# Kernel optimization log

Hardware: AMD Instinct MI355X
Metric: run time of the kernel (lower is better)

## Reference

```python
import jax, jax.numpy as jnp
import numpy as np

GROUPS = 32
EPS = 1e-5


def group_norm(x, gamma, beta):
    # x: [B,H,W,C], channels_last, groups over channel dim (Keras GroupNormalization default)
    B, H, W, C = x.shape
    xg = x.reshape(B, H, W, GROUPS, C // GROUPS)
    mean = xg.mean(axis=(1, 2, 4), keepdims=True)
    var = xg.var(axis=(1, 2, 4), keepdims=True)
    xn = ((xg - mean) * jax.lax.rsqrt(var + EPS)).reshape(B, H, W, C)
    return xn * gamma + beta


def conv1x1(x, w, b):
    # 1x1 conv == per-pixel dense: [B,H,W,C] x [C,D] -> [B,H,W,D]
    return jnp.einsum('bhwc,cd->bhwd', x, w) + b


def setup_inputs() -> dict:
    key = jax.random.key(0)
    ks = jax.random.split(key, 10)
    C = 512
    s = 1.0 / np.sqrt(C)
    inp = {
        'x': jax.random.normal(ks[0], (2, 64, 64, C), dtype=jnp.float32),
        'gamma': jnp.ones((C,), jnp.float32),
        'beta': jnp.zeros((C,), jnp.float32),
        'wq': jax.random.normal(ks[1], (C, C), jnp.float32) * s,
        'bq': jnp.zeros((C,), jnp.float32),
        'wk': jax.random.normal(ks[2], (C, C), jnp.float32) * s,
        'bk': jnp.zeros((C,), jnp.float32),
        'wv': jax.random.normal(ks[3], (C, C), jnp.float32) * s,
        'bv': jnp.zeros((C,), jnp.float32),
        'wp': jax.random.normal(ks[4], (C, C), jnp.float32) * s,
        'bp': jnp.zeros((C,), jnp.float32),
    }
    return inp


def reference(x, gamma, beta, wq, bq, wk, bk, wv, bv, wp, bp):
    B, H, W, C = x.shape
    N = H * W
    xn = group_norm(x, gamma, beta)
    q = conv1x1(xn, wq, bq).reshape(B, N, C)
    k = conv1x1(xn, wk, bk).reshape(B, N, C)
    v = conv1x1(xn, wv, bv).reshape(B, N, C)
    scale = 1.0 / jnp.sqrt(jnp.asarray(C, x.dtype))
    scores = jnp.einsum('bnc,bmc->bnm', q, k) * scale  # [B,N,N]
    attn = jax.nn.softmax(scores, axis=-1)
    out = jnp.einsum('bnm,bmc->bnc', attn, v).reshape(B, H, W, C)
    return conv1x1(out, wp, bp) + x
```

## Files before the change

kernel.cpp:

```cpp
#include <hip/hip_runtime.h>
#include <hip/hip_fp16.h>

typedef _Float16 half_t;
typedef _Float16 half8 __attribute__((ext_vector_type(8)));
typedef float floatx4 __attribute__((ext_vector_type(4)));

static constexpr int BATCH = 2;
static constexpr int NSP = 4096;
static constexpr int CH = 512;
static constexpr int NQKV = 3 * CH;
static constexpr int KSPLIT = 4;

static constexpr size_t OFF_STATS = 0;
static constexpr size_t OFF_ROWSUM = 512;
static constexpr size_t OFF_PST = 33280;
static constexpr size_t OFF_WQKV = 196608;
static constexpr size_t WQKV_BYTES = (size_t)NQKV * CH * 2;
static constexpr size_t OFF_WP = OFF_WQKV + WQKV_BYTES;
static constexpr size_t WP_BYTES = (size_t)CH * CH * 2;
static constexpr size_t OFF_XN = OFF_WP + WP_BYTES;
static constexpr size_t XN_BYTES = (size_t)BATCH * NSP * CH * 2;
static constexpr size_t OFF_QKV = OFF_XN + XN_BYTES;
static constexpr size_t QKV_BYTES = (size_t)BATCH * NSP * NQKV * 2;
static constexpr size_t OFF_VT = OFF_QKV + QKV_BYTES;
static constexpr size_t OFF_AO = OFF_VT + XN_BYTES;
static constexpr size_t OFF_S = OFF_AO + XN_BYTES;
static constexpr size_t S_BYTES_1 = (size_t)NSP * NSP * 2;
static constexpr size_t OFF_PART = OFF_XN;

__device__ __forceinline__ void gld16(void* lds, const void* g) {
  __builtin_amdgcn_global_load_lds(
      (__attribute__((address_space(1))) void*)(g),
      (__attribute__((address_space(3))) void*)(lds),
      16, 0, 0);
}

__global__ __launch_bounds__(256) void gn_stats(const float* __restrict__ x,
                                                float* __restrict__ pst) {
  int b = blockIdx.y;
  int tid = (int)threadIdx.x;
  int g = ((tid * 4) & (CH - 1)) >> 4;
  const float* base = x + (long)b * NSP * CH + (long)blockIdx.x * 16 * CH + tid * 4;
  float s = 0.f, s2 = 0.f;
#pragma unroll
  for (int it = 0; it < 8; ++it) {
    floatx4 v = *(const floatx4*)(base + (long)it * 1024);
#pragma unroll
    for (int r = 0; r < 4; ++r) { s += v[r]; s2 += v[r] * v[r]; }
  }
  __shared__ float gs[32], gs2[32];
  if (tid < 32) { gs[tid] = 0.f; gs2[tid] = 0.f; }
  __syncthreads();
  atomicAdd(&gs[g], s);
  atomicAdd(&gs2[g], s2);
  __syncthreads();
  if (tid < 32) {
    long idx = ((long)(b * 256 + blockIdx.x) * 32 + tid) * 2;
    pst[idx] = gs[tid];
    pst[idx + 1] = gs2[tid];
  }
}

__global__ __launch_bounds__(256) void gn_finalize(const float* __restrict__ pst,
                                                   float* __restrict__ st,
                                                   float* __restrict__ rowsum) {
  int tid = (int)threadIdx.x;
  int bg = tid & 63;
  int p = tid >> 6;
  int b = bg >> 5, g = bg & 31;
  float s = 0.f, s2 = 0.f;
  for (int j = 0; j < 64; ++j) {
    int chunk = p * 64 + j;
    long idx = ((long)(b * 256 + chunk) * 32 + g) * 2;
    s += pst[idx];
    s2 += pst[idx + 1];
  }
  __shared__ float rs[64][4], rs2[64][4];
  rs[bg][p] = s;
  rs2[bg][p] = s2;
  __syncthreads();
  if (tid < 64) {
    float ts = rs[tid][0] + rs[tid][1] + rs[tid][2] + rs[tid][3];
    float ts2 = rs2[tid][0] + rs2[tid][1] + rs2[tid][2] + rs2[tid][3];
    const float inv = 1.f / 65536.f;
    float mean = ts * inv;
    float var = ts2 * inv - mean * mean;
    st[tid * 2] = mean;
    st[tid * 2 + 1] = rsqrtf(var + 1e-5f);
  }
  floatx4* rz = (floatx4*)rowsum;
#pragma unroll
  for (int j = 0; j < 8; ++j)
    rz[tid + j * 256] = floatx4{0.f, 0.f, 0.f, 0.f};
}

__global__ __launch_bounds__(256) void gn_apply(const float* __restrict__ x,
                                                const float* __restrict__ st,
                                                const float* __restrict__ gamma,
                                                const float* __restrict__ beta,
                                                half_t* __restrict__ xn) {
  long i = ((long)blockIdx.x * 256 + threadIdx.x) * 8;
  int c = (int)(i & (CH - 1));
  int b = (int)(i >> 21);
  int g = c >> 4;
  float mean = st[((b << 5) + g) * 2];
  float rstd = st[((b << 5) + g) * 2 + 1];
  floatx4 a = *(const floatx4*)(x + i);
  floatx4 d = *(const floatx4*)(x + i + 4);
  half8 o;
#pragma unroll
  for (int r = 0; r < 4; ++r) {
    o[r]     = (half_t)((a[r] - mean) * rstd * gamma[c + r] + beta[c + r]);
    o[r + 4] = (half_t)((d[r] - mean) * rstd * gamma[c + r + 4] + beta[c + r + 4]);
  }
  *(half8*)(xn + i) = o;
}

__global__ __launch_bounds__(256) void transpose_w(
    const float* __restrict__ w0, const float* __restrict__ w1,
    const float* __restrict__ w2, const float* __restrict__ w3,
    half_t* __restrict__ o0, half_t* __restrict__ o1,
    half_t* __restrict__ o2, half_t* __restrict__ o3) {
  const float* w; half_t* o;
  switch (blockIdx.z) {
    case 0: w = w0; o = o0; break;
    case 1: w = w1; o = o1; break;
    case 2: w = w2; o = o2; break;
    default: w = w3; o = o3; break;
  }
  __shared__ float t[32][33];
  int d0 = blockIdx.x * 32, c0 = blockIdx.y * 32;
  int tx = threadIdx.x & 31, ty = threadIdx.x >> 5;
#pragma unroll
  for (int i = 0; i < 4; ++i)
    t[ty + i * 8][tx] = w[(long)(c0 + ty + i * 8) * CH + d0 + tx];
  __syncthreads();
#pragma unroll
  for (int i = 0; i < 4; ++i) {
    int d = ty + i * 8;
    o[(long)(d0 + d) * CH + c0 + tx] = (half_t)t[tx][d];
  }
}

__global__ __launch_bounds__(256) void transpose_v(const half_t* __restrict__ v,
                                                   half_t* __restrict__ vt) {
  __shared__ half_t t[32][33];
  int b = blockIdx.z;
  int d0 = blockIdx.x * 32, n0 = blockIdx.y * 32;
  int tx = threadIdx.x & 31, ty = threadIdx.x >> 5;
  const half_t* vb = v + (long)b * NSP * NQKV;
  half_t* ob = vt + (long)b * NSP * CH;
#pragma unroll
  for (int i = 0; i < 4; ++i)
    t[ty + i * 8][tx] = vb[(long)(n0 + ty + i * 8) * NQKV + d0 + tx];
  __syncthreads();
#pragma unroll
  for (int i = 0; i < 4; ++i) {
    int d = ty + i * 8;
    ob[(long)(d0 + d) * NSP + n0 + tx] = t[tx][d];
  }
}

template <int BM, int BN, int BK, int EPI, int SWZ, int KSP, typename OutT>
__global__ __launch_bounds__(256) void gemm_nt(
    const half_t* __restrict__ X, const half_t* __restrict__ Y,
    OutT* __restrict__ Co, const float* __restrict__ b0,
    const float* __restrict__ b1, const float* __restrict__ b2,
    const float* __restrict__ resid, float* __restrict__ rowsum,
    int M, int N, int K, int ldx, int ldy, int ldc,
    long xbs, long ybs, long cbs, float scale) {
  constexpr int SM = BM / 32;
  constexpr int SN = BN / 32;
  constexpr int ROWS = BM + BN;
  constexpr int CPR = BK / 8;
  constexpr int RPW = 64 / CPR;
  constexpr int ROUNDS = (ROWS * BK * 2) / 4096;
  constexpr int KSTEPS = BK / 32;
  static_assert(BM % (4 * RPW) == 0, "no As/Bs straddle within a round");
  __shared__ __align__(16) half_t Sh[ROWS * BK];

  const int zb = blockIdx.z / KSP;
  const int ks = blockIdx.z % KSP;
  int bx, by;
  if (SWZ == 1) {
    int lin = (int)(blockIdx.x + gridDim.x * blockIdx.y);
    int wmt = 256 / (int)gridDim.x;
    by = wmt * (lin >> 8) + ((lin & 255) % wmt);
    bx = (lin & 255) / wmt;
  } else if (SWZ == 2) {
    by = blockIdx.x;
    bx = blockIdx.y;
  } else {
    bx = blockIdx.x;
    by = blockIdx.y;
  }

  const half_t* Xb = X + (long)zb * xbs + (long)ks * K;
  const half_t* Yb = Y + (long)zb * ybs + (long)ks * K;
  OutT* Cb = Co + (long)blockIdx.z * cbs;

  const int m0 = by * BM;
  const int n0 = bx * BN;
  const int tid = (int)threadIdx.x;
  const int wave = tid >> 6;
  const int lane = tid & 63;
  const int quad = lane >> 4;
  const int l16 = lane & 15;
  const int wm = wave >> 1;
  const int wn = wave & 1;

  floatx4 acc[SM][SN] = {};

  const int srow = lane / CPR;
  const int schunk = lane % CPR;
  const char* Xc = (const char*)Xb;

  int soff[ROUNDS];
#pragma unroll
  for (int r = 0; r < ROUNDS; ++r) {
    int row = r * (4 * RPW) + wave * RPW + srow;
    int gchunk = schunk ^ (row & (CPR - 1));
    const char* p = (row < BM)
        ? (const char*)(Xb + (long)(m0 + row) * ldx)
        : (const char*)(Yb + (long)(n0 + row - BM) * ldy);
    soff[r] = (int)(p + gchunk * 16 - Xc);
  }

  int offA[SM], offB[SN];
#pragma unroll
  for (int i = 0; i < SM; ++i) {
    int m = wm * (BM / 2) + i * 16 + l16;
    int cc = quad ^ (m & (CPR - 1));
    offA[i] = (m * BK + cc * 8) * 2;
  }
#pragma unroll
  for (int j = 0; j < SN; ++j) {
    int n = wn * (BN / 2) + j * 16 + l16;
    int cc = quad ^ (n & (CPR - 1));
    offB[j] = (BM * BK + n * BK + cc * 8) * 2;
  }

  for (int k0 = 0; k0 < K; k0 += BK) {
#pragma unroll
    for (int r = 0; r < ROUNDS; ++r) {
      gld16((char*)Sh + (r * 4 + wave) * 1024, Xc + (long)soff[r]);
      soff[r] += BK * 2;
    }
    __syncthreads();

#pragma unroll
    for (int kk = 0; kk < KSTEPS; ++kk) {
      const int kx = kk << 6;
      half8 af[SM], bf[SN];
#pragma unroll
      for (int i = 0; i < SM; ++i)
        af[i] = *(const half8*)((const char*)Sh + (offA[i] ^ kx));
#pragma unroll
      for (int j = 0; j < SN; ++j)
        bf[j] = *(const half8*)((const char*)Sh + (offB[j] ^ kx));
#pragma unroll
      for (int i = 0; i < SM; ++i)
#pragma unroll
        for (int j = 0; j < SN; ++j)
          acc[i][j] = __builtin_amdgcn_mfma_f32_16x16x32_f16(af[i], bf[j], acc[i][j], 0, 0, 0);
    }
    __syncthreads();
  }

#pragma unroll
  for (int i = 0; i < SM; ++i) {
    int gmb = m0 + wm * (BM / 2) + i * 16 + quad * 4;
    float rs[4] = {0.f, 0.f, 0.f, 0.f};
#pragma unroll
    for (int j = 0; j < SN; ++j) {
      int gn = n0 + wn * (BN / 2) + j * 16 + l16;
      float bias = 0.f, sc = 1.f;
      if (EPI == 1) {
        if (gn < CH) { bias = b0[gn]; sc = scale; }
        else if (gn < 2 * CH) { bias = b1[gn - CH]; }
        else { bias = b2[gn - 2 * CH]; }
      } else if (EPI == 2) {
        bias = b0[gn];
      }
#pragma unroll
      for (int r = 0; r < 4; ++r) {
        long idx = (long)(gmb + r) * ldc + gn;
        float v = acc[i][j][r];
        if (EPI == 1) v = (v + bias) * sc;
        if (EPI == 2) v = v + bias + resid[idx];
        if (EPI == 3) { v = __expf(v); rs[r] += v; }
        Cb[idx] = (OutT)v;
      }
    }
    if (EPI == 3) {
#pragma unroll
      for (int r = 0; r < 4; ++r) {
        float v = rs[r];
        v += __shfl_xor(v, 1);
        v += __shfl_xor(v, 2);
        v += __shfl_xor(v, 4);
        v += __shfl_xor(v, 8);
        if (l16 == 0) atomicAdd(&rowsum[(long)zb * NSP + gmb + r], v);
      }
    }
  }
}

__global__ __launch_bounds__(256) void pv_combine(const half_t* __restrict__ part,
                                                  const float* __restrict__ rowsum,
                                                  half_t* __restrict__ ao) {
  const long bNC = (long)NSP * CH;
  long i = ((long)blockIdx.x * 256 + threadIdx.x) * 8;
  int b = (int)(i >> 21);
  long inner = i & ((1L << 21) - 1);
  float inv = 1.f / rowsum[i >> 9];
  float s[8] = {};
#pragma unroll
  for (int ks = 0; ks < KSPLIT; ++ks) {
    half8 h = *(const half8*)(part + ((long)(b * KSPLIT + ks)) * bNC + inner);
#pragma unroll
    for (int r = 0; r < 8; ++r) s[r] += (float)h[r];
  }
  half8 o;
#pragma unroll
  for (int r = 0; r < 8; ++r) o[r] = (half_t)(s[r] * inv);
  *(half8*)(ao + i) = o;
}

extern "C" void kernel_launch(void* const* d_in, const int* in_sizes, int n_in,
                              void* d_out, int out_size, void* d_ws, size_t ws_size,
                              hipStream_t stream) {
  const float* x = (const float*)d_in[0];
  const float* gamma = (const float*)d_in[1];
  const float* beta = (const float*)d_in[2];
  const float* wq = (const float*)d_in[3];
  const float* bq = (const float*)d_in[4];
  const float* wk = (const float*)d_in[5];
  const float* bk = (const float*)d_in[6];
  const float* wv = (const float*)d_in[7];
  const float* bv = (const float*)d_in[8];
  const float* wp = (const float*)d_in[9];
  const float* bp = (const float*)d_in[10];
  float* out = (float*)d_out;
  char* ws = (char*)d_ws;

  float* st = (float*)(ws + OFF_STATS);
  float* rsum = (float*)(ws + OFF_ROWSUM);
  float* pst = (float*)(ws + OFF_PST);
  half_t* wqkvT = (half_t*)(ws + OFF_WQKV);
  half_t* wpT = (half_t*)(ws + OFF_WP);
  half_t* xn = (half_t*)(ws + OFF_XN);
  half_t* qkv = (half_t*)(ws + OFF_QKV);
  half_t* vt = (half_t*)(ws + OFF_VT);
  half_t* ao = (half_t*)(ws + OFF_AO);
  half_t* S = (half_t*)(ws + OFF_S);
  half_t* part = (half_t*)(ws + OFF_PART);

  half_t* q = qkv;
  half_t* k = qkv + CH;
  half_t* v = qkv + 2 * CH;

  const float scale = 0.044194173824159216f;
  const long bQKV = (long)NSP * NQKV;
  const long bNC = (long)NSP * CH;
  const long bNN = (long)NSP * NSP;

  gn_stats<<<dim3(256, BATCH), 256, 0, stream>>>(x, pst);
  gn_finalize<<<1, 256, 0, stream>>>(pst, st, rsum);
  gn_apply<<<2048, 256, 0, stream>>>(x, st, gamma, beta, xn);
  transpose_w<<<dim3(16, 16, 4), 256, 0, stream>>>(
      wq, wk, wv, wp, wqkvT, wqkvT + (size_t)CH * CH, wqkvT + 2 * (size_t)CH * CH, wpT);

  gemm_nt<128, 128, 64, 1, 2, 1, half_t><<<dim3(BATCH * NSP / 128, NQKV / 128, 1), 256, 0, stream>>>(
      xn, wqkvT, qkv, bq, bk, bv, nullptr, nullptr, BATCH * NSP, NQKV, CH,
      CH, CH, NQKV, 0, 0, 0, scale);
  transpose_v<<<dim3(16, 128, BATCH), 256, 0, stream>>>(v, vt);

  bool full = ws_size >= OFF_S + 2 * S_BYTES_1;
  if (full) {
    gemm_nt<128, 128, 64, 3, 1, 1, half_t><<<dim3(32, 32, BATCH), 256, 0, stream>>>(
        q, k, S, nullptr, nullptr, nullptr, nullptr, rsum, NSP, NSP, CH,
        NQKV, NQKV, NSP, bQKV, bQKV, bNN, 1.f);
    gemm_nt<128, 128, 64, 0, 2, KSPLIT, half_t><<<dim3(NSP / 128, CH / 128, BATCH * KSPLIT), 256, 0, stream>>>(
        S, vt, part, nullptr, nullptr, nullptr, nullptr, nullptr, NSP, CH, NSP / KSPLIT,
        NSP, NSP, CH, bNN, bNC, bNC, 1.f);
    pv_combine<<<2048, 256, 0, stream>>>(part, rsum, ao);
  } else {
    for (int bb = 0; bb < BATCH; ++bb) {
      gemm_nt<128, 128, 64, 3, 1, 1, half_t><<<dim3(32, 32, 1), 256, 0, stream>>>(
          q + bb * bQKV, k + bb * bQKV, S, nullptr, nullptr, nullptr, nullptr,
          rsum + bb * NSP, NSP, NSP, CH, NQKV, NQKV, NSP, 0, 0, 0, 1.f);
      gemm_nt<128, 128, 64, 0, 2, KSPLIT, half_t><<<dim3(NSP / 128, CH / 128, KSPLIT), 256, 0, stream>>>(
          S, vt + bb * bNC, part + (long)bb * KSPLIT * bNC, nullptr, nullptr, nullptr,
          nullptr, nullptr, NSP, CH, NSP / KSPLIT, NSP, NSP, CH, 0, 0, bNC, 1.f);
    }
    pv_combine<<<2048, 256, 0, stream>>>(part, rsum, ao);
  }
  gemm_nt<64, 64, 128, 2, 2, 1, float><<<dim3(BATCH * NSP / 64, CH / 64, 1), 256, 0, stream>>>(
      ao, wpT, out, bp, nullptr, nullptr, x, nullptr, BATCH * NSP, CH, CH,
      CH, CH, CH, 0, 0, 0, 1.f);
}
```

Before: 257.3 us.

## Add 256x256 eight-wave pipelined GEMM for attention QK and PV stages

Adds a new GEMM kernel with 256x256 tiles, 512 threads and a 128 KB LDS double buffer. Direct global-to-LDS loads are interleaved with MFMA phases, controlled by explicit vmcnt waits, barriers and setprio. The QK^T (with exp and rowsum epilogue) and split-K PV GEMMs now use it instead of the 128x128 kernel. The aim is more data reuse per tile and better overlap of loads with compute. In exchange, fewer blocks are launched, LDS use is very large, and the hand-tuned wait counts must be exactly right to stay correct.

```diff
diff --git a/kernel.cpp b/kernel.cpp
--- a/kernel.cpp
+++ b/kernel.cpp
@@ -34,6 +34,13 @@
       (__attribute__((address_space(3))) void*)(lds),
       16, 0, 0);
 }
+
+#define VMCNT(n) asm volatile("s_waitcnt vmcnt(" #n ")" ::: "memory")
+#define LGKM0()                                         \
+  do {                                                  \
+    asm volatile("s_waitcnt lgkmcnt(0)" ::: "memory");  \
+    __builtin_amdgcn_sched_barrier(0);                  \
+  } while (0)
 
 __global__ __launch_bounds__(256) void gn_stats(const float* __restrict__ x,
                                                 float* __restrict__ pst) {
@@ -306,6 +313,157 @@
   }
 }
 
+template <int EPI, int KSP, typename OutT>
+__global__ __launch_bounds__(512, 2) void gemm8p(
+    const half_t* __restrict__ X, const half_t* __restrict__ Y,
+    OutT* __restrict__ Co, float* __restrict__ rowsum,
+    int K, int ldx, int ldy, int ldc, long xbs, long ybs, long cbs) {
+  __shared__ __align__(16) char smem[131072];
+  const int zb = (int)blockIdx.z / KSP;
+  const int ks = (int)blockIdx.z % KSP;
+  const int m0 = (int)blockIdx.x * 256;
+  const int n0 = (int)blockIdx.y * 256;
+  const int tid = (int)threadIdx.x;
+  const int w = tid >> 6;
+  const int l = tid & 63;
+  const int quad = l >> 4;
+  const int l16 = l & 15;
+  const int wm = w >> 2;
+  const int wn = w & 3;
+
+  const half_t* Xb = X + (long)zb * xbs + (long)ks * K;
+  const half_t* Yb = Y + (long)zb * ybs + (long)ks * K;
+  OutT* Cb = Co + (long)blockIdx.z * cbs;
+  const char* Xc = (const char*)Xb;
+
+  int soff[8];
+  {
+    const int lr = l >> 3;
+    const int g = (l & 7) ^ (lr & 7);
+#pragma unroll
+    for (int r = 0; r < 8; ++r) {
+      const int R = (r * 8 + w) * 8 + lr;
+      const char* p = (R < 256)
+          ? (const char*)(Xb + (long)(m0 + R) * ldx)
+          : (const char*)(Yb + (long)(n0 + R - 256) * ldy);
+      soff[r] = (int)(p + g * 16 - Xc);
+    }
+  }
+
+  int offA[8], offB[4];
+#pragma unroll
+  for (int i = 0; i < 8; ++i) {
+    const int m = wm * 128 + i * 16 + l16;
+    offA[i] = m * 128 + ((quad ^ (m & 7)) << 4);
+  }
+#pragma unroll
+  for (int j = 0; j < 4; ++j) {
+    const int n = wn * 64 + j * 16 + l16;
+    offB[j] = 32768 + n * 128 + ((quad ^ (n & 7)) << 4);
+  }
+
+  floatx4 acc[8][4] = {};
+
+#pragma unroll
+  for (int r = 0; r < 8; ++r) {
+    gld16(smem + (r * 8 + w) * 1024, Xc + (long)soff[r]);
+    soff[r] += 128;
+  }
+  {
+    constexpr int pr[6] = {4, 5, 6, 7, 0, 2};
+#pragma unroll
+    for (int t = 0; t < 6; ++t) {
+      gld16(smem + 65536 + (pr[t] * 8 + w) * 1024, Xc + (long)soff[pr[t]]);
+      soff[pr[t]] += 128;
+    }
+  }
+  VMCNT(6);
+  __builtin_amdgcn_s_barrier();
+
+  const int NI = K >> 7;
+  half8 bf[4][2];
+  for (int it = 0; it < NI; ++it) {
+    const bool last = (it == NI - 1);
+    constexpr int sr0[8] = {1, 4, 6, 0, 1, 4, 6, 0};
+    constexpr int sr1[8] = {3, 5, 7, 2, 3, 5, 7, 2};
+    constexpr int spar[8] = {1, 0, 0, 0, 0, 1, 1, 1};
+#pragma unroll
+    for (int ph = 0; ph < 8; ++ph) {
+      const int q = ph & 3;
+      const char* bb = smem + (ph >> 2) * 65536;
+      if (q == 0) {
+#pragma unroll
+        for (int j = 0; j < 4; ++j)
+#pragma unroll
+          for (int kk = 0; kk < 2; ++kk)
+            bf[j][kk] = *(const half8*)(bb + (offB[j] ^ (kk << 6)));
+      }
+      half8 af[2][2];
+#pragma unroll
+      for (int i2 = 0; i2 < 2; ++i2)
+#pragma unroll
+        for (int kk = 0; kk < 2; ++kk)
+          af[i2][kk] = *(const half8*)(bb + (offA[q * 2 + i2] ^ (kk << 6)));
+      if (ph == 0 || !last) {
+        const int r0 = sr0[ph], r1 = sr1[ph];
+        char* db = smem + spar[ph] * 65536;
+        gld16(db + (r0 * 8 + w) * 1024, Xc + (long)soff[r0]);
+        soff[r0] += 128;
+        gld16(db + (r1 * 8 + w) * 1024, Xc + (long)soff[r1]);
+        soff[r1] += 128;
+      }
+      __builtin_amdgcn_s_barrier();
+      LGKM0();
+      __builtin_amdgcn_s_setprio(1);
+#pragma unroll
+      for (int i2 = 0; i2 < 2; ++i2)
+#pragma unroll
+        for (int j = 0; j < 4; ++j)
+#pragma unroll
+          for (int kk = 0; kk < 2; ++kk)
+            acc[q * 2 + i2][j] = __builtin_amdgcn_mfma_f32_16x16x32_f16(
+                af[i2][kk], bf[j][kk], acc[q * 2 + i2][j], 0, 0, 0);
+      __builtin_amdgcn_s_setprio(0);
+      if (ph == 3) {
+        if (last) { VMCNT(2); } else { VMCNT(8); }
+      } else if (ph == 5) {
+        if (last) { VMCNT(0); } else { VMCNT(10); }
+      } else if (ph == 7) {
+        if (!last) { VMCNT(6); }
+      }
+      __builtin_amdgcn_s_barrier();
+    }
+  }
+
+#pragma unroll
+  for (int i = 0; i < 8; ++i) {
+    const int gmb = m0 + wm * 128 + i * 16 + quad * 4;
+    float rs[4] = {0.f, 0.f, 0.f, 0.f};
+#pragma unroll
+    for (int j = 0; j < 4; ++j) {
+      const int gn = n0 + wn * 64 + j * 16 + l16;
+#pragma unroll
+      for (int r = 0; r < 4; ++r) {
+        long idx = (long)(gmb + r) * ldc + gn;
+        float v = acc[i][j][r];
+        if (EPI == 3) { v = __expf(v); rs[r] += v; }
+        Cb[idx] = (OutT)v;
+      }
+    }
+    if (EPI == 3) {
+#pragma unroll
+      for (int r = 0; r < 4; ++r) {
+        float v = rs[r];
+        v += __shfl_xor(v, 1);
+        v += __shfl_xor(v, 2);
+        v += __shfl_xor(v, 4);
+        v += __shfl_xor(v, 8);
+        if (l16 == 0) atomicAdd(&rowsum[(long)zb * NSP + gmb + r], v);
+      }
+    }
+  }
+}
+
 __global__ __launch_bounds__(256) void pv_combine(const half_t* __restrict__ part,
                                                   const float* __restrict__ rowsum,
                                                   half_t* __restrict__ ao) {
@@ -378,21 +536,19 @@
 
   bool full = ws_size >= OFF_S + 2 * S_BYTES_1;
   if (full) {
-    gemm_nt<128, 128, 64, 3, 1, 1, half_t><<<dim3(32, 32, BATCH), 256, 0, stream>>>(
-        q, k, S, nullptr, nullptr, nullptr, nullptr, rsum, NSP, NSP, CH,
-        NQKV, NQKV, NSP, bQKV, bQKV, bNN, 1.f);
-    gemm_nt<128, 128, 64, 0, 2, KSPLIT, half_t><<<dim3(NSP / 128, CH / 128, BATCH * KSPLIT), 256, 0, stream>>>(
-        S, vt, part, nullptr, nullptr, nullptr, nullptr, nullptr, NSP, CH, NSP / KSPLIT,
-        NSP, NSP, CH, bNN, bNC, bNC, 1.f);
+    gemm8p<3, 1, half_t><<<dim3(NSP / 256, NSP / 256, BATCH), 512, 0, stream>>>(
+        q, k, S, rsum, CH, NQKV, NQKV, NSP, bQKV, bQKV, bNN);
+    gemm8p<0, KSPLIT, half_t><<<dim3(NSP / 256, CH / 256, BATCH * KSPLIT), 512, 0, stream>>>(
+        S, vt, part, nullptr, NSP / KSPLIT, NSP, NSP, CH, bNN, bNC, bNC);
     pv_combine<<<2048, 256, 0, stream>>>(part, rsum, ao);
   } else {
     for (int bb = 0; bb < BATCH; ++bb) {
-      gemm_nt<128, 128, 64, 3, 1, 1, half_t><<<dim3(32, 32, 1), 256, 0, stream>>>(
-          q + bb * bQKV, k + bb * bQKV, S, nullptr, nullptr, nullptr, nullptr,
-          rsum + bb * NSP, NSP, NSP, CH, NQKV, NQKV, NSP, 0, 0, 0, 1.f);
-      gemm_nt<128, 128, 64, 0, 2, KSPLIT, half_t><<<dim3(NSP / 128, CH / 128, KSPLIT), 256, 0, stream>>>(
-          S, vt + bb * bNC, part + (long)bb * KSPLIT * bNC, nullptr, nullptr, nullptr,
-          nullptr, nullptr, NSP, CH, NSP / KSPLIT, NSP, NSP, CH, 0, 0, bNC, 1.f);
+      gemm8p<3, 1, half_t><<<dim3(NSP / 256, NSP / 256, 1), 512, 0, stream>>>(
+          q + bb * bQKV, k + bb * bQKV, S, rsum + bb * NSP, CH,
+          NQKV, NQKV, NSP, 0, 0, 0);
+      gemm8p<0, KSPLIT, half_t><<<dim3(NSP / 256, CH / 256, KSPLIT), 512, 0, stream>>>(
+          S, vt + bb * bNC, part + (long)bb * KSPLIT * bNC, nullptr,
+          NSP / KSPLIT, NSP, NSP, CH, 0, 0, bNC);
     }
     pv_combine<<<2048, 256, 0, stream>>>(part, rsum, ao);
   }
```

New measurement: 239.1 us. 1.08x faster.

## Fuse QK^T, exp and PV into a single flash-style attention kernel

Applied to the files above, without the earlier changes.

Replaces the two-GEMM attention path, which wrote the full N×N exponentiated score matrix to global memory, with one kernel. Each workgroup computes a 128-row score tile, exponentiates it into LDS, and multiplies by V^T while accumulating row sums. Q/K/V tiles are loaded with direct-to-LDS global loads, double-buffered and synchronised by hand with waitcnt/barriers and setprio. This removes the large S write/read traffic and one launch. In exchange it uses 128 KB of LDS per block and a complex manual pipeline, which limits occupancy and carries synchronisation risk.

```diff
diff --git a/kernel.cpp b/kernel.cpp
--- a/kernel.cpp
+++ b/kernel.cpp
@@ -25,8 +25,7 @@
 static constexpr size_t OFF_VT = OFF_QKV + QKV_BYTES;
 static constexpr size_t OFF_AO = OFF_VT + XN_BYTES;
 static constexpr size_t OFF_S = OFF_AO + XN_BYTES;
-static constexpr size_t S_BYTES_1 = (size_t)NSP * NSP * 2;
-static constexpr size_t OFF_PART = OFF_XN;
+static constexpr size_t OFF_PART = OFF_S;
 
 __device__ __forceinline__ void gld16(void* lds, const void* g) {
   __builtin_amdgcn_global_load_lds(
@@ -34,6 +33,13 @@
       (__attribute__((address_space(3))) void*)(lds),
       16, 0, 0);
 }
+
+#define VMCNT(n) asm volatile("s_waitcnt vmcnt(" #n ")" ::: "memory")
+#define LGKM0()                                         \
+  do {                                                  \
+    asm volatile("s_waitcnt lgkmcnt(0)" ::: "memory");  \
+    __builtin_amdgcn_sched_barrier(0);                  \
+  } while (0)
 
 __global__ __launch_bounds__(256) void gn_stats(const float* __restrict__ x,
                                                 float* __restrict__ pst) {
@@ -270,7 +276,6 @@
 #pragma unroll
   for (int i = 0; i < SM; ++i) {
     int gmb = m0 + wm * (BM / 2) + i * 16 + quad * 4;
-    float rs[4] = {0.f, 0.f, 0.f, 0.f};
 #pragma unroll
     for (int j = 0; j < SN; ++j) {
       int gn = n0 + wn * (BN / 2) + j * 16 + l16;
@@ -288,20 +293,207 @@
         float v = acc[i][j][r];
         if (EPI == 1) v = (v + bias) * sc;
         if (EPI == 2) v = v + bias + resid[idx];
-        if (EPI == 3) { v = __expf(v); rs[r] += v; }
         Cb[idx] = (OutT)v;
       }
     }
-    if (EPI == 3) {
-#pragma unroll
-      for (int r = 0; r < 4; ++r) {
-        float v = rs[r];
-        v += __shfl_xor(v, 1);
-        v += __shfl_xor(v, 2);
-        v += __shfl_xor(v, 4);
-        v += __shfl_xor(v, 8);
-        if (l16 == 0) atomicAdd(&rowsum[(long)zb * NSP + gmb + r], v);
+  }
+}
+
+__global__ __launch_bounds__(512, 2) void fattn(
+    const half_t* __restrict__ Q, const half_t* __restrict__ Kp,
+    const half_t* __restrict__ VT, half_t* __restrict__ part,
+    float* __restrict__ rowsum) {
+  __shared__ __align__(16) char smem[131072];
+  const int zb = (int)blockIdx.x >> 5;
+  const int mt = (int)blockIdx.x & 31;
+  const int ksp = (int)blockIdx.y;
+  const int m0 = mt * 128;
+  const int kv0 = ksp * (NSP / KSPLIT);
+  const int tid = (int)threadIdx.x;
+  const int w = tid >> 6;
+  const int l = tid & 63;
+  const int quad = l >> 4;
+  const int l16 = l & 15;
+  const int wm = w >> 2;
+  const int wn = w & 3;
+  const int wd = w & 3;
+
+  const char* Qc = (const char*)(Q + (long)zb * NSP * NQKV);
+  const char* Kc = (const char*)(Kp + (long)zb * NSP * NQKV);
+  const char* Vc = (const char*)(VT + (long)zb * NSP * CH);
+
+  int soffQ, soffK, soffV[4];
+  {
+    const int lu = l >> 3, le = l & 7;
+    int u = w * 8 + lu;
+    int e = le ^ (u & 7);
+    int R = (u << 1) | (e >> 2);
+    soffQ = ((m0 + R) * NQKV + (e & 3) * 8) * 2;
+    u = 64 + w * 8 + lu;
+    e = le ^ (u & 7);
+    R = ((u << 1) | (e >> 2)) - 128;
+    soffK = ((kv0 + R) * NQKV + (e & 3) * 8) * 2;
+#pragma unroll
+    for (int r = 0; r < 4; ++r) {
+      u = r * 64 + w * 8 + lu;
+      e = le ^ (u & 7);
+      R = (u << 1) | (e >> 2);
+      soffV[r] = (R * NSP + kv0 + (e & 3) * 8) * 2;
+    }
+  }
+
+  int offA[4], offB[2], offV[8], offP0[4];
+#pragma unroll
+  for (int i = 0; i < 4; ++i) {
+    const int R = wm * 64 + i * 16 + l16;
+    offA[i] = (R >> 1) * 128 + (((((R & 1) << 2) | quad) ^ ((R >> 1) & 7)) << 4);
+    offP0[i] = 98304 + R * 256 + ((quad ^ (R & 15)) << 4);
+  }
+#pragma unroll
+  for (int j = 0; j < 2; ++j) {
+    const int R = 128 + wn * 32 + j * 16 + l16;
+    offB[j] = (R >> 1) * 128 + (((((R & 1) << 2) | quad) ^ ((R >> 1) & 7)) << 4);
+  }
+#pragma unroll
+  for (int jj = 0; jj < 8; ++jj) {
+    const int R = wd * 128 + jj * 16 + l16;
+    offV[jj] = (R >> 1) * 128 + (((((R & 1) << 2) | quad) ^ ((R >> 1) & 7)) << 4);
+  }
+
+  floatx4 acc_o[4][8] = {};
+  float rs[4][4] = {};
+
+  gld16(smem + w * 1024, Qc + (long)soffQ);
+  gld16(smem + (8 + w) * 1024, Kc + (long)soffK);
+  soffQ += 64; soffK += 64;
+  VMCNT(0);
+  __builtin_amdgcn_s_barrier();
+
+  for (int it = 0; it < 8; ++it) {
+    floatx4 acc_s[4][2] = {};
+#pragma unroll
+    for (int ks = 0; ks < 16; ++ks) {
+      const char* scur = smem + (ks & 1) * 16384;
+      if (ks < 15) {
+        char* sn = smem + ((ks + 1) & 1) * 16384;
+        gld16(sn + w * 1024, Qc + (long)soffQ);
+        gld16(sn + (8 + w) * 1024, Kc + (long)soffK);
+        soffQ += 64; soffK += 64;
+      } else {
+        char* vn = smem + 32768;
+#pragma unroll
+        for (int r = 0; r < 4; ++r) {
+          gld16(vn + (r * 8 + w) * 1024, Vc + (long)soffV[r]);
+          soffV[r] += 64;
+        }
       }
+      half8 af[4], bf[2];
+#pragma unroll
+      for (int i = 0; i < 4; ++i) af[i] = *(const half8*)(scur + offA[i]);
+#pragma unroll
+      for (int j = 0; j < 2; ++j) bf[j] = *(const half8*)(scur + offB[j]);
+      LGKM0();
+      __builtin_amdgcn_s_setprio(1);
+#pragma unroll
+      for (int i = 0; i < 4; ++i)
+#pragma unroll
+        for (int j = 0; j < 2; ++j)
+          acc_s[i][j] = __builtin_amdgcn_mfma_f32_16x16x32_f16(af[i], bf[j], acc_s[i][j], 0, 0, 0);
+      __builtin_amdgcn_s_setprio(0);
+      VMCNT(0);
+      __builtin_amdgcn_s_barrier();
+    }
+    soffQ -= 1024;
+    soffK += 128 * NQKV * 2 - 1024;
+#pragma unroll
+    for (int i = 0; i < 4; ++i) {
+      const int mrow = wm * 64 + i * 16 + quad * 4;
+#pragma unroll
+      for (int j = 0; j < 2; ++j) {
+        const int n = wn * 32 + j * 16 + l16;
+        const int cw = n >> 3;
+        const int nlo = (n & 7) * 2;
+#pragma unroll
+        for (int r = 0; r < 4; ++r) {
+          float v = __expf(acc_s[i][j][r]);
+          rs[i][r] += v;
+          const int m = mrow + r;
+          *(half_t*)(smem + 98304 + m * 256 + (((cw ^ (m & 15)) << 4) | nlo)) = (half_t)v;
+        }
+      }
+    }
+    LGKM0();
+    __builtin_amdgcn_s_barrier();
+#pragma unroll
+    for (int pk = 0; pk < 4; ++pk) {
+      const char* vcur = smem + 32768 + (pk & 1) * 32768;
+      if (pk < 3) {
+        char* vn = smem + 32768 + ((pk + 1) & 1) * 32768;
+#pragma unroll
+        for (int r = 0; r < 4; ++r) {
+          gld16(vn + (r * 8 + w) * 1024, Vc + (long)soffV[r]);
+          soffV[r] += 64;
+        }
+      } else if (it < 7) {
+        gld16(smem + w * 1024, Qc + (long)soffQ);
+        gld16(smem + (8 + w) * 1024, Kc + (long)soffK);
+        soffQ += 64; soffK += 64;
+      }
+      half8 paf[4], vb0[4];
+#pragma unroll
+      for (int i = 0; i < 4; ++i)
+        paf[i] = *(const half8*)(smem + (offP0[i] ^ (pk << 6)));
+#pragma unroll
+      for (int jj = 0; jj < 4; ++jj)
+        vb0[jj] = *(const half8*)(vcur + offV[jj]);
+      LGKM0();
+      __builtin_amdgcn_s_setprio(1);
+#pragma unroll
+      for (int jj = 0; jj < 4; ++jj)
+#pragma unroll
+        for (int i = 0; i < 4; ++i)
+          acc_o[i][jj] = __builtin_amdgcn_mfma_f32_16x16x32_f16(paf[i], vb0[jj], acc_o[i][jj], 0, 0, 0);
+      __builtin_amdgcn_s_setprio(0);
+      half8 vb1[4];
+#pragma unroll
+      for (int jj = 0; jj < 4; ++jj)
+        vb1[jj] = *(const half8*)(vcur + offV[4 + jj]);
+      LGKM0();
+      __builtin_amdgcn_s_setprio(1);
+#pragma unroll
+      for (int jj = 0; jj < 4; ++jj)
+#pragma unroll
+        for (int i = 0; i < 4; ++i)
+          acc_o[i][4 + jj] = __builtin_amdgcn_mfma_f32_16x16x32_f16(paf[i], vb1[jj], acc_o[i][4 + jj], 0, 0, 0);
+      __builtin_amdgcn_s_setprio(0);
+      VMCNT(0);
+      __builtin_amdgcn_s_barrier();
+    }
+  }
+
+#pragma unroll
+  for (int i = 0; i < 4; ++i)
+#pragma unroll
+    for (int r = 0; r < 4; ++r) {
+      float v = rs[i][r];
+      v += __shfl_xor(v, 1);
+      v += __shfl_xor(v, 2);
+      v += __shfl_xor(v, 4);
+      v += __shfl_xor(v, 8);
+      if (l16 == 0)
+        atomicAdd(&rowsum[(long)zb * NSP + m0 + wm * 64 + i * 16 + quad * 4 + r], v);
+    }
+
+  half_t* pb = part + ((long)(zb * KSPLIT + ksp)) * NSP * CH;
+#pragma unroll
+  for (int i = 0; i < 4; ++i) {
+    const int gm = m0 + wm * 64 + i * 16 + quad * 4;
+#pragma unroll
+    for (int jj = 0; jj < 8; ++jj) {
+      const int gd = wd * 128 + jj * 16 + l16;
+#pragma unroll
+      for (int r = 0; r < 4; ++r)
+        pb[(long)(gm + r) * CH + gd] = (half_t)acc_o[i][jj][r];
     }
   }
 }
@@ -353,7 +545,6 @@
   half_t* qkv = (half_t*)(ws + OFF_QKV);
   half_t* vt = (half_t*)(ws + OFF_VT);
   half_t* ao = (half_t*)(ws + OFF_AO);
-  half_t* S = (half_t*)(ws + OFF_S);
   half_t* part = (half_t*)(ws + OFF_PART);
 
   half_t* q = qkv;
@@ -361,9 +552,6 @@
   half_t* v = qkv + 2 * CH;
 
   const float scale = 0.044194173824159216f;
-  const long bQKV = (long)NSP * NQKV;
-  const long bNC = (long)NSP * CH;
-  const long bNN = (long)NSP * NSP;
 
   gn_stats<<<dim3(256, BATCH), 256, 0, stream>>>(x, pst);
   gn_finalize<<<1, 256, 0, stream>>>(pst, st, rsum);
@@ -376,26 +564,9 @@
       CH, CH, NQKV, 0, 0, 0, scale);
   transpose_v<<<dim3(16, 128, BATCH), 256, 0, stream>>>(v, vt);
 
-  bool full = ws_size >= OFF_S + 2 * S_BYTES_1;
-  if (full) {
-    gemm_nt<128, 128, 64, 3, 1, 1, half_t><<<dim3(32, 32, BATCH), 256, 0, stream>>>(
-        q, k, S, nullptr, nullptr, nullptr, nullptr, rsum, NSP, NSP, CH,
-        NQKV, NQKV, NSP, bQKV, bQKV, bNN, 1.f);
-    gemm_nt<128, 128, 64, 0, 2, KSPLIT, half_t><<<dim3(NSP / 128, CH / 128, BATCH * KSPLIT), 256, 0, stream>>>(
-        S, vt, part, nullptr, nullptr, nullptr, nullptr, nullptr, NSP, CH, NSP / KSPLIT,
-        NSP, NSP, CH, bNN, bNC, bNC, 1.f);
-    pv_combine<<<2048, 256, 0, stream>>>(part, rsum, ao);
-  } else {
-    for (int bb = 0; bb < BATCH; ++bb) {
-      gemm_nt<128, 128, 64, 3, 1, 1, half_t><<<dim3(32, 32, 1), 256, 0, stream>>>(
-          q + bb * bQKV, k + bb * bQKV, S, nullptr, nullptr, nullptr, nullptr,
-          rsum + bb * NSP, NSP, NSP, CH, NQKV, NQKV, NSP, 0, 0, 0, 1.f);
-      gemm_nt<128, 128, 64, 0, 2, KSPLIT, half_t><<<dim3(NSP / 128, CH / 128, KSPLIT), 256, 0, stream>>>(
-          S, vt + bb * bNC, part + (long)bb * KSPLIT * bNC, nullptr, nullptr, nullptr,
-          nullptr, nullptr, NSP, CH, NSP / KSPLIT, NSP, NSP, CH, 0, 0, bNC, 1.f);
-    }
-    pv_combine<<<2048, 256, 0, stream>>>(part, rsum, ao);
-  }
+  fattn<<<dim3(BATCH * NSP / 128, KSPLIT), 512, 0, stream>>>(q, k, vt, part, rsum);
+  pv_combine<<<2048, 256, 0, stream>>>(part, rsum, ao);
+
   gemm_nt<64, 64, 128, 2, 2, 1, float><<<dim3(BATCH * NSP / 64, CH / 64, 1), 256, 0, stream>>>(
       ao, wpT, out, bp, nullptr, nullptr, x, nullptr, BATCH * NSP, CH, CH,
       CH, CH, CH, 0, 0, 0, 1.f);
```

New measurement: 327.0 us. +27.1%, slower.
